# Performance work log

Measured on AMD Instinct MI355X. Metric: run time of the kernel, lower is better.

Reference implementation:

```python
import jax, jax.numpy as jnp
import numpy as np

N_NODES = 50000
N_EDGES = 800000
D_FEAT = 128


def setup_inputs() -> dict:
    key = jax.random.key(0)
    k1, k2, k3, k4 = jax.random.split(key, 4)
    h = jax.random.normal(k1, (N_NODES, D_FEAT), dtype=jnp.float32)
    w = jax.random.normal(k2, (N_EDGES,), dtype=jnp.float32)  # per-edge scalar weight
    src = jax.random.randint(k3, (N_EDGES,), 0, N_NODES, dtype=jnp.int32)
    dst = jax.random.randint(k4, (N_EDGES,), 0, N_NODES, dtype=jnp.int32)
    return {"h": h, "w": w, "src": src, "dst": dst}


def reference(h, w, src, dst):
    # Edge-weighted message passing (u_mul_e + mean reduce), then concat [h, h_N].
    n_nodes = h.shape[0]
    msg = h[src] * w[:, None]                                  # [E, F] gather + scale
    agg = jax.ops.segment_sum(msg, dst, num_segments=n_nodes)  # [N, F] scatter-add
    ones = jnp.ones((msg.shape[0],), dtype=h.dtype)
    deg = jax.ops.segment_sum(ones, dst, num_segments=n_nodes) # in-degree per node
    h_N = agg / jnp.maximum(deg, 1.0)[:, None]                 # mean over incoming edges
    return jnp.concatenate([h, h_N], axis=1)                   # [N, 2F]
```

## Files before the change

### kernel.cpp

```cpp
#include <hip/hip_runtime.h>
#include <hip/hip_fp16.h>

#define D_FEAT 128
#define SHIFT 7
#define NPB   128
#define CAPB  3072
#define NBMAX 512
#define EPT   8
#define CAST_BLOCKS 1536


__global__ void __launch_bounds__(256) fused_cast_bucket_kernel(
    const float* __restrict__ h, __half* __restrict__ hb,
    float* __restrict__ out, int n_elems,
    const float* __restrict__ w, const int* __restrict__ src,
    const int* __restrict__ dst,
    int* __restrict__ bcur, int2* __restrict__ buck, int n_edges,
    int fill_blocks, int nb)
{
    __shared__ int lcnt[NBMAX];
    __shared__ int lbase[NBMAX];
    __shared__ int lpos[NBMAX];
    if ((int)blockIdx.x < fill_blocks) {
        const int t  = threadIdx.x;
        const int cb = blockIdx.x * (256 * EPT);
        for (int bb = t; bb < NBMAX; bb += 256) { lcnt[bb] = 0; lpos[bb] = 0; }
        __syncthreads();
        int ed[EPT], es[EPT]; float ew[EPT];
#pragma unroll
        for (int j = 0; j < EPT; ++j) {
            const int e = cb + j * 256 + t;
            if (e < n_edges) {
                ed[j] = dst[e]; es[j] = src[e]; ew[j] = w[e];
                atomicAdd(&lcnt[ed[j] >> SHIFT], 1);
            } else ed[j] = -1;
        }
        __syncthreads();
        for (int bb = t; bb < nb; bb += 256) {
            const int c = lcnt[bb];
            lbase[bb] = c ? atomicAdd(&bcur[bb], c) : 0;
        }
        __syncthreads();
#pragma unroll
        for (int j = 0; j < EPT; ++j) {
            if (ed[j] >= 0) {
                const int b   = ed[j] >> SHIFT;
                const unsigned lid = (unsigned)(ed[j] & (NPB - 1));
                const int p   = atomicAdd(&lpos[b], 1);
                const int gp  = lbase[b] + p;
                if (gp < CAPB)
                    buck[(size_t)b * CAPB + gp] =
                        make_int2((int)((lid << 24) | (unsigned)es[j]), __float_as_int(ew[j]));
            }
        }
    } else {
        const int t      = (blockIdx.x - fill_blocks) * 256 + threadIdx.x;
        const int stride = CAST_BLOCKS * 256;
        const int n4     = n_elems >> 2;
        for (int i = t; i < n4; i += stride) {
            const float4 v = ((const float4*)h)[i];
            ((__half2*)hb)[2 * i]     = __float22half2_rn(make_float2(v.x, v.y));
            ((__half2*)hb)[2 * i + 1] = __float22half2_rn(make_float2(v.z, v.w));
            const int n = i >> 5;
            const int q = i & 31;
            ((float4*)(out + (size_t)n * 2 * D_FEAT))[q] = v;
        }
    }
}

__global__ void __launch_bounds__(1024) bucket_gather_kernel(
    const int* __restrict__ bcur, const int2* __restrict__ buck,
    const __half* __restrict__ hb, float* __restrict__ out, int n_nodes)
{
    __shared__ int2 ebuf[CAPB];
    __shared__ int2 ebuf2[CAPB];
    __shared__ int  ncnt[NPB];
    __shared__ int  sst[NPB];
    __shared__ int  ncur[NPB];
    const int b = blockIdx.x;
    const int t = threadIdx.x;
    const size_t base = (size_t)b * CAPB;
    int cnt = bcur[b]; if (cnt > CAPB) cnt = CAPB;

    if (t < NPB) ncnt[t] = 0;
    __syncthreads();
    for (int i = t; i < cnt; i += 1024) {
        const int2 e = buck[base + i];
        ebuf[i] = e;
        atomicAdd(&ncnt[((unsigned)e.x) >> 24], 1);
    }
    __syncthreads();
    int v = 0;
    if (t < NPB) { v = ncnt[t]; sst[t] = v; }
    __syncthreads();
    for (int o = 1; o < NPB; o <<= 1) {
        int x = 0;
        if (t < NPB && t >= o) x = sst[t - o];
        __syncthreads();
        if (t < NPB) sst[t] += x;
        __syncthreads();
    }
    if (t < NPB) { const int st = sst[t] - v; sst[t] = st; ncur[t] = st; }
    __syncthreads();
    for (int i = t; i < cnt; i += 1024) {
        const int2 e = ebuf[i];
        const unsigned ex = (unsigned)e.x;
        const int lid = (int)(ex >> 24);
        const int p = atomicAdd(&ncur[lid], 1);
        ebuf2[p] = make_int2((int)(ex & 0xFFFFFFu), e.y);
    }
    __syncthreads();

    const int lane = t & 63;
    const int wv   = t >> 6;

#define HROW(s) __half22float2(((const __half2*)(hb + (size_t)(s) * D_FEAT))[lane])

    for (int ln = wv; ln < NPB; ln += 16) {
        const int n = b * NPB + ln;
        if (n >= n_nodes) continue;
        const int st = sst[ln];
        const int c  = ncnt[ln];
        float2 acc = make_float2(0.0f, 0.0f);
        int k = 0;
        for (; k + 8 <= c; k += 8) {
            const int2 b0 = ebuf2[st + k + 0], b1 = ebuf2[st + k + 1];
            const int2 b2 = ebuf2[st + k + 2], b3 = ebuf2[st + k + 3];
            const int2 b4 = ebuf2[st + k + 4], b5 = ebuf2[st + k + 5];
            const int2 b6 = ebuf2[st + k + 6], b7 = ebuf2[st + k + 7];
            const float2 h0 = HROW(b0.x);
            const float2 h1 = HROW(b1.x);
            const float2 h2 = HROW(b2.x);
            const float2 h3 = HROW(b3.x);
            const float2 h4 = HROW(b4.x);
            const float2 h5 = HROW(b5.x);
            const float2 h6 = HROW(b6.x);
            const float2 h7 = HROW(b7.x);
            const float w0 = __int_as_float(b0.y), w1 = __int_as_float(b1.y);
            const float w2 = __int_as_float(b2.y), w3 = __int_as_float(b3.y);
            const float w4 = __int_as_float(b4.y), w5 = __int_as_float(b5.y);
            const float w6 = __int_as_float(b6.y), w7 = __int_as_float(b7.y);
            acc.x = fmaf(h0.x, w0, acc.x); acc.y = fmaf(h0.y, w0, acc.y);
            acc.x = fmaf(h1.x, w1, acc.x); acc.y = fmaf(h1.y, w1, acc.y);
            acc.x = fmaf(h2.x, w2, acc.x); acc.y = fmaf(h2.y, w2, acc.y);
            acc.x = fmaf(h3.x, w3, acc.x); acc.y = fmaf(h3.y, w3, acc.y);
            acc.x = fmaf(h4.x, w4, acc.x); acc.y = fmaf(h4.y, w4, acc.y);
            acc.x = fmaf(h5.x, w5, acc.x); acc.y = fmaf(h5.y, w5, acc.y);
            acc.x = fmaf(h6.x, w6, acc.x); acc.y = fmaf(h6.y, w6, acc.y);
            acc.x = fmaf(h7.x, w7, acc.x); acc.y = fmaf(h7.y, w7, acc.y);
        }
        for (; k < c; ++k) {
            const int2 e = ebuf2[st + k];
            const float ww = __int_as_float(e.y);
            const float2 hv = HROW(e.x);
            acc.x = fmaf(hv.x, ww, acc.x);
            acc.y = fmaf(hv.y, ww, acc.y);
        }
        const float inv = 1.0f / fmaxf((float)c, 1.0f);
        float2* orow = (float2*)(out + (size_t)n * 2 * D_FEAT + D_FEAT);
        orow[lane] = make_float2(acc.x * inv, acc.y * inv);
    }
#undef HROW
}


#define CAP 32
#define T2_CAST_BLOCKS 512
#define T2_FILL_BLOCKS 2048

__global__ void __launch_bounds__(256) fused_cast_fill_kernel(
    const float* __restrict__ h, __half* __restrict__ hb,
    float* __restrict__ out, int n_elems,
    const float* __restrict__ w, const int* __restrict__ src,
    const int* __restrict__ dst,
    int* __restrict__ count, int* __restrict__ ovf_count,
    int* __restrict__ ovf_list, int2* __restrict__ bins, int n_edges)
{
    if (blockIdx.x < T2_CAST_BLOCKS) {
        const int t      = blockIdx.x * blockDim.x + threadIdx.x;
        const int stride = T2_CAST_BLOCKS * blockDim.x;
        const int n4     = n_elems >> 2;
        for (int i = t; i < n4; i += stride) {
            const float4 v = ((const float4*)h)[i];
            ((__half2*)hb)[2 * i]     = __float22half2_rn(make_float2(v.x, v.y));
            ((__half2*)hb)[2 * i + 1] = __float22half2_rn(make_float2(v.z, v.w));
            const int n = i >> 5;
            const int q = i & 31;
            ((float4*)(out + (size_t)n * 2 * D_FEAT))[q] = v;
        }
    } else {
        const int t      = (blockIdx.x - T2_CAST_BLOCKS) * blockDim.x + threadIdx.x;
        const int stride = T2_FILL_BLOCKS * blockDim.x;
        for (int e = t; e < n_edges; e += stride) {
            const int d = dst[e];
            const int pos = atomicAdd(&count[d], 1);
            if (pos < CAP) {
                bins[(size_t)d * CAP + pos] = make_int2(src[e], __float_as_int(w[e]));
            } else {
                const int o = atomicAdd(ovf_count, 1);
                ovf_list[o] = e;
            }
        }
    }
}

__global__ void __launch_bounds__(256) t2_gather_kernel(
    const __half* __restrict__ hb, const int* __restrict__ count,
    const int2* __restrict__ bins, float* __restrict__ out, int n_nodes)
{
    const int lane = threadIdx.x & 63;
    const int wave = (blockIdx.x * blockDim.x + threadIdx.x) >> 6;
    if (wave >= n_nodes) return;
    const int n   = wave;
    const int cnt = count[n];
    const int c   = cnt < CAP ? cnt : CAP;
    float2 acc = make_float2(0.0f, 0.0f);
    const int2* bp = bins + (size_t)n * CAP;
    for (int k = 0; k < c; ++k) {
        const int2 b = bp[k];
        const float2 hv = __half22float2(((const __half2*)(hb + (size_t)b.x * D_FEAT))[lane]);
        const float ww = __int_as_float(b.y);
        acc.x = fmaf(hv.x, ww, acc.x);
        acc.y = fmaf(hv.y, ww, acc.y);
    }
    const float inv = 1.0f / fmaxf((float)cnt, 1.0f);
    float2* orow = (float2*)(out + (size_t)n * 2 * D_FEAT + D_FEAT);
    orow[lane] = make_float2(acc.x * inv, acc.y * inv);
}

__global__ void __launch_bounds__(256) overflow_kernel(
    const __half* __restrict__ hb, const float* __restrict__ w,
    const int* __restrict__ src, const int* __restrict__ dst,
    const int* __restrict__ count, const int* __restrict__ ovf_count,
    const int* __restrict__ ovf_list, float* __restrict__ out)
{
    const int novf = *ovf_count;
    if (novf == 0) return;
    const int lane  = threadIdx.x & 63;
    const int wave  = (blockIdx.x * blockDim.x + threadIdx.x) >> 6;
    const int nwave = (gridDim.x * blockDim.x) >> 6;
    for (int idx = wave; idx < novf; idx += nwave) {
        const int e = ovf_list[idx];
        const int s = src[e];
        const int d = dst[e];
        const float scale = w[e] / fmaxf((float)count[d], 1.0f);
        const float2 hv = __half22float2(((const __half2*)(hb + (size_t)s * D_FEAT))[lane]);
        float* od = out + (size_t)d * 2 * D_FEAT + D_FEAT + (lane << 1);
        atomicAdd(od,     hv.x * scale);
        atomicAdd(od + 1, hv.y * scale);
    }
}


__global__ void __launch_bounds__(256) edge_scatter_kernel(
    const float* __restrict__ h, const float* __restrict__ w,
    const int* __restrict__ src, const int* __restrict__ dst,
    float* __restrict__ out, float* __restrict__ deg, int n_edges)
{
    const int lane  = threadIdx.x & 63;
    const int wave  = (blockIdx.x * blockDim.x + threadIdx.x) >> 6;
    const int nwave = (gridDim.x * blockDim.x) >> 6;
    for (int e = wave; e < n_edges; e += nwave) {
        const int   s  = src[e];
        const int   d  = dst[e];
        const float we = w[e];
        const float2 hv = ((const float2*)(h + (size_t)s * D_FEAT))[lane];
        float* od = out + (size_t)d * (2 * D_FEAT) + D_FEAT + (lane << 1);
        atomicAdd(od,     hv.x * we);
        atomicAdd(od + 1, hv.y * we);
        if (lane == 0) atomicAdd(deg + d, 1.0f);
    }
}

__global__ void __launch_bounds__(256) finalize_kernel(
    const float* __restrict__ h, const float* __restrict__ deg,
    float* __restrict__ out, int n_nodes)
{
    int i = blockIdx.x * blockDim.x + threadIdx.x;
    const int total  = n_nodes * 32;
    const int stride = gridDim.x * blockDim.x;
    for (; i < total; i += stride) {
        const int n = i >> 5;
        const int q = i & 31;
        const float4 hv = ((const float4*)(h + (size_t)n * D_FEAT))[q];
        ((float4*)(out + (size_t)n * 2 * D_FEAT))[q] = hv;
        const float inv = 1.0f / fmaxf(deg[n], 1.0f);
        float4* ap = ((float4*)(out + (size_t)n * 2 * D_FEAT + D_FEAT)) + q;
        float4 a = *ap;
        a.x *= inv; a.y *= inv; a.z *= inv; a.w *= inv;
        *ap = a;
    }
}


extern "C" void kernel_launch(void* const* d_in, const int* in_sizes, int n_in,
                              void* d_out, int out_size, void* d_ws, size_t ws_size,
                              hipStream_t stream) {
    const float* h   = (const float*)d_in[0];
    const float* w   = (const float*)d_in[1];
    const int*   src = (const int*)d_in[2];
    const int*   dst = (const int*)d_in[3];
    float* out = (float*)d_out;

    const int n_edges = in_sizes[1];
    const int n_nodes = in_sizes[0] / D_FEAT;
    const int n_hel   = in_sizes[0];
    const int NB      = (n_nodes + NPB - 1) >> SHIFT;

    const size_t bcur_b = NBMAX * sizeof(int);
    const size_t bk_b   = (size_t)NB * CAPB * sizeof(int2);
    const size_t hb_b   = (size_t)n_hel * sizeof(__half);
    const size_t need1  = bcur_b + bk_b + hb_b;

    const size_t t2_count_b = (size_t)(n_nodes + 16) * sizeof(int);
    const size_t t2_bins_b  = (size_t)n_nodes * CAP * sizeof(int2);
    const size_t t2_ovf_b   = (size_t)n_edges * sizeof(int);
    const size_t need2      = t2_count_b + t2_bins_b + t2_ovf_b + hb_b;

    if (ws_size >= need1 && NB <= NBMAX) {
        char* p = (char*)d_ws;
        int*    bcur = (int*)p;      p += bcur_b;
        int2*   buck = (int2*)p;     p += bk_b;
        __half* hb   = (__half*)p;

        const int fill_blocks = (n_edges + 256 * EPT - 1) / (256 * EPT);
        (void)hipMemsetAsync(bcur, 0, bcur_b, stream);
        fused_cast_bucket_kernel<<<fill_blocks + CAST_BLOCKS, 256, 0, stream>>>(
            h, hb, out, n_hel, w, src, dst, bcur, buck, n_edges, fill_blocks, NB);
        bucket_gather_kernel<<<NB, 1024, 0, stream>>>(bcur, buck, hb, out, n_nodes);
    } else if (ws_size >= need2) {
        int*    count     = (int*)d_ws;
        int*    ovf_count = count + n_nodes;
        int2*   bins      = (int2*)((char*)d_ws + t2_count_b);
        int*    ovf_list  = (int*)((char*)d_ws + t2_count_b + t2_bins_b);
        __half* hb        = (__half*)((char*)d_ws + t2_count_b + t2_bins_b + t2_ovf_b);

        (void)hipMemsetAsync(count, 0, t2_count_b, stream);
        fused_cast_fill_kernel<<<T2_CAST_BLOCKS + T2_FILL_BLOCKS, 256, 0, stream>>>(
            h, hb, out, n_hel, w, src, dst, count, ovf_count, ovf_list, bins, n_edges);
        t2_gather_kernel<<<(n_nodes + 3) / 4, 256, 0, stream>>>(hb, count, bins, out, n_nodes);
        overflow_kernel<<<64, 256, 0, stream>>>(hb, w, src, dst, count, ovf_count,
                                                ovf_list, out);
    } else {
        float* deg = (float*)d_ws;
        (void)hipMemsetAsync(out, 0, (size_t)out_size * sizeof(float), stream);
        (void)hipMemsetAsync(deg, 0, (size_t)n_nodes * sizeof(float), stream);
        edge_scatter_kernel<<<2048, 256, 0, stream>>>(h, w, src, dst, out, deg, n_edges);
        finalize_kernel<<<2048, 256, 0, stream>>>(h, deg, out, n_nodes);
    }
}
```

Baseline: 65.93 us.

## Split half-precision features into four column panels for cache-friendly gather

The fp16 copy of h is now stored as four feature panels of 32 columns each, laid out node-major inside each panel. The gather kernel walks the panels one after another, so each pass only touches a quarter of the feature table and that slice has a better chance of staying in cache. Within a pass, a wavefront splits into four 16-lane groups that each fetch a different edge's 64-byte slice, and the partial sums are combined with shuffles. The cost is four passes over each node's edge list, extra shuffle reductions, and predicated loads in the tail iterations.

```diff
diff --git a/kernel.cpp b/kernel.cpp
--- a/kernel.cpp
+++ b/kernel.cpp
@@ -11,8 +11,8 @@
 
 
 __global__ void __launch_bounds__(256) fused_cast_bucket_kernel(
-    const float* __restrict__ h, __half* __restrict__ hb,
-    float* __restrict__ out, int n_elems,
+    const float* __restrict__ h, __half* __restrict__ hbt,
+    float* __restrict__ out, int n_elems, int n_nodes,
     const float* __restrict__ w, const int* __restrict__ src,
     const int* __restrict__ dst,
     int* __restrict__ bcur, int2* __restrict__ buck, int n_edges,
@@ -59,10 +59,13 @@
         const int n4     = n_elems >> 2;
         for (int i = t; i < n4; i += stride) {
             const float4 v = ((const float4*)h)[i];
-            ((__half2*)hb)[2 * i]     = __float22half2_rn(make_float2(v.x, v.y));
-            ((__half2*)hb)[2 * i + 1] = __float22half2_rn(make_float2(v.z, v.w));
             const int n = i >> 5;
             const int q = i & 31;
+            const int p = q >> 3;
+            const int fo = (q & 7) << 1;
+            __half2* hp = (__half2*)hbt + ((size_t)p * n_nodes + n) * 16 + fo;
+            hp[0] = __float22half2_rn(make_float2(v.x, v.y));
+            hp[1] = __float22half2_rn(make_float2(v.z, v.w));
             ((float4*)(out + (size_t)n * 2 * D_FEAT))[q] = v;
         }
     }
@@ -70,7 +73,7 @@
 
 __global__ void __launch_bounds__(1024) bucket_gather_kernel(
     const int* __restrict__ bcur, const int2* __restrict__ buck,
-    const __half* __restrict__ hb, float* __restrict__ out, int n_nodes)
+    const __half* __restrict__ hbt, float* __restrict__ out, int n_nodes)
 {
     __shared__ int2 ebuf[CAPB];
     __shared__ int2 ebuf2[CAPB];
@@ -113,54 +116,47 @@
 
     const int lane = t & 63;
     const int wv   = t >> 6;
-
-#define HROW(s) __half22float2(((const __half2*)(hb + (size_t)(s) * D_FEAT))[lane])
-
-    for (int ln = wv; ln < NPB; ln += 16) {
-        const int n = b * NPB + ln;
-        if (n >= n_nodes) continue;
-        const int st = sst[ln];
-        const int c  = ncnt[ln];
-        float2 acc = make_float2(0.0f, 0.0f);
-        int k = 0;
-        for (; k + 8 <= c; k += 8) {
-            const int2 b0 = ebuf2[st + k + 0], b1 = ebuf2[st + k + 1];
-            const int2 b2 = ebuf2[st + k + 2], b3 = ebuf2[st + k + 3];
-            const int2 b4 = ebuf2[st + k + 4], b5 = ebuf2[st + k + 5];
-            const int2 b6 = ebuf2[st + k + 6], b7 = ebuf2[st + k + 7];
-            const float2 h0 = HROW(b0.x);
-            const float2 h1 = HROW(b1.x);
-            const float2 h2 = HROW(b2.x);
-            const float2 h3 = HROW(b3.x);
-            const float2 h4 = HROW(b4.x);
-            const float2 h5 = HROW(b5.x);
-            const float2 h6 = HROW(b6.x);
-            const float2 h7 = HROW(b7.x);
-            const float w0 = __int_as_float(b0.y), w1 = __int_as_float(b1.y);
-            const float w2 = __int_as_float(b2.y), w3 = __int_as_float(b3.y);
-            const float w4 = __int_as_float(b4.y), w5 = __int_as_float(b5.y);
-            const float w6 = __int_as_float(b6.y), w7 = __int_as_float(b7.y);
-            acc.x = fmaf(h0.x, w0, acc.x); acc.y = fmaf(h0.y, w0, acc.y);
-            acc.x = fmaf(h1.x, w1, acc.x); acc.y = fmaf(h1.y, w1, acc.y);
-            acc.x = fmaf(h2.x, w2, acc.x); acc.y = fmaf(h2.y, w2, acc.y);
-            acc.x = fmaf(h3.x, w3, acc.x); acc.y = fmaf(h3.y, w3, acc.y);
-            acc.x = fmaf(h4.x, w4, acc.x); acc.y = fmaf(h4.y, w4, acc.y);
-            acc.x = fmaf(h5.x, w5, acc.x); acc.y = fmaf(h5.y, w5, acc.y);
-            acc.x = fmaf(h6.x, w6, acc.x); acc.y = fmaf(h6.y, w6, acc.y);
-            acc.x = fmaf(h7.x, w7, acc.x); acc.y = fmaf(h7.y, w7, acc.y);
-        }
-        for (; k < c; ++k) {
-            const int2 e = ebuf2[st + k];
-            const float ww = __int_as_float(e.y);
-            const float2 hv = HROW(e.x);
-            acc.x = fmaf(hv.x, ww, acc.x);
-            acc.y = fmaf(hv.y, ww, acc.y);
-        }
-        const float inv = 1.0f / fmaxf((float)c, 1.0f);
-        float2* orow = (float2*)(out + (size_t)n * 2 * D_FEAT + D_FEAT);
-        orow[lane] = make_float2(acc.x * inv, acc.y * inv);
-    }
-#undef HROW
+    const int g    = lane >> 4;
+    const int fl   = lane & 15;
+
+    for (int p = 0; p < 4; ++p) {
+        const __half2* __restrict__ hp = (const __half2*)hbt + (size_t)p * n_nodes * 16;
+        for (int ln = wv; ln < NPB; ln += 16) {
+            const int n = b * NPB + ln;
+            if (n >= n_nodes) continue;
+            const int st = sst[ln];
+            const int c  = ncnt[ln];
+            float2 acc = make_float2(0.f, 0.f);
+            for (int k = 0; k < c; k += 16) {
+                const int j0 = k + g, j1 = k + 4 + g, j2 = k + 8 + g, j3 = k + 12 + g;
+                const int2 e0 = ebuf2[st + (j0 < c ? j0 : 0)];
+                const int2 e1 = ebuf2[st + (j1 < c ? j1 : 0)];
+                const int2 e2 = ebuf2[st + (j2 < c ? j2 : 0)];
+                const int2 e3 = ebuf2[st + (j3 < c ? j3 : 0)];
+                const float w0 = j0 < c ? __int_as_float(e0.y) : 0.f;
+                const float w1 = j1 < c ? __int_as_float(e1.y) : 0.f;
+                const float w2 = j2 < c ? __int_as_float(e2.y) : 0.f;
+                const float w3 = j3 < c ? __int_as_float(e3.y) : 0.f;
+                const float2 h0 = __half22float2(hp[(size_t)e0.x * 16 + fl]);
+                const float2 h1 = __half22float2(hp[(size_t)e1.x * 16 + fl]);
+                const float2 h2 = __half22float2(hp[(size_t)e2.x * 16 + fl]);
+                const float2 h3 = __half22float2(hp[(size_t)e3.x * 16 + fl]);
+                acc.x = fmaf(h0.x, w0, acc.x); acc.y = fmaf(h0.y, w0, acc.y);
+                acc.x = fmaf(h1.x, w1, acc.x); acc.y = fmaf(h1.y, w1, acc.y);
+                acc.x = fmaf(h2.x, w2, acc.x); acc.y = fmaf(h2.y, w2, acc.y);
+                acc.x = fmaf(h3.x, w3, acc.x); acc.y = fmaf(h3.y, w3, acc.y);
+            }
+            acc.x += __shfl_xor(acc.x, 16, 64);
+            acc.y += __shfl_xor(acc.y, 16, 64);
+            acc.x += __shfl_xor(acc.x, 32, 64);
+            acc.y += __shfl_xor(acc.y, 32, 64);
+            if (g == 0) {
+                const float inv = 1.0f / fmaxf((float)c, 1.0f);
+                float2* op = (float2*)(out + (size_t)n * 2 * D_FEAT + D_FEAT + p * 32) + fl;
+                *op = make_float2(acc.x * inv, acc.y * inv);
+            }
+        }
+    }
 }
 
 
@@ -317,17 +313,17 @@
     const size_t t2_ovf_b   = (size_t)n_edges * sizeof(int);
     const size_t need2      = t2_count_b + t2_bins_b + t2_ovf_b + hb_b;
 
-    if (ws_size >= need1 && NB <= NBMAX) {
+    if (ws_size >= need1 && NB <= NBMAX && (in_sizes[0] % D_FEAT) == 0) {
         char* p = (char*)d_ws;
         int*    bcur = (int*)p;      p += bcur_b;
         int2*   buck = (int2*)p;     p += bk_b;
-        __half* hb   = (__half*)p;
+        __half* hbt  = (__half*)p;
 
         const int fill_blocks = (n_edges + 256 * EPT - 1) / (256 * EPT);
         (void)hipMemsetAsync(bcur, 0, bcur_b, stream);
         fused_cast_bucket_kernel<<<fill_blocks + CAST_BLOCKS, 256, 0, stream>>>(
-            h, hb, out, n_hel, w, src, dst, bcur, buck, n_edges, fill_blocks, NB);
-        bucket_gather_kernel<<<NB, 1024, 0, stream>>>(bcur, buck, hb, out, n_nodes);
+            h, hbt, out, n_hel, n_nodes, w, src, dst, bcur, buck, n_edges, fill_blocks, NB);
+        bucket_gather_kernel<<<NB, 1024, 0, stream>>>(bcur, buck, hbt, out, n_nodes);
     } else if (ws_size >= need2) {
         int*    count     = (int*)d_ws;
         int*    ovf_count = count + n_nodes;
```

After: 94.51 us. 1.43x slower.
